# Kernel optimization log

Hardware: AMD Instinct MI355X
Metric: run time of the kernel (lower is better)

The kernel has to match this reference:

```python
import jax, jax.numpy as jnp
import numpy as np

RES_SCALE = 1.0

def prelu(x, a):
    return jnp.maximum(x, 0) + a * jnp.minimum(x, 0)

def conv1x1_prelu(x, w, b, a):
    # x: [N,C,H,W], w: [O,C], b: [O]
    y = jnp.einsum('nchw,oc->nohw', x, w) + b[None, :, None, None]
    return prelu(y, a)

def setup_inputs() -> dict:
    key = jax.random.key(0)
    ks = jax.random.split(key, 5)
    N, C, H, W = 2, 128, 96, 96
    Cr = C // 2  # reduction = 2
    return {
        'x':  jax.random.normal(ks[0], (N, C, H, W), jnp.float32),
        'w1': jax.random.normal(ks[1], (Cr, C), jnp.float32) * (1.0 / np.sqrt(C)),
        'b1': jnp.zeros((Cr,), jnp.float32),
        'a1': jnp.asarray(0.25, jnp.float32),
        'w2': jax.random.normal(ks[2], (Cr, C), jnp.float32) * (1.0 / np.sqrt(C)),
        'b2': jnp.zeros((Cr,), jnp.float32),
        'a2': jnp.asarray(0.25, jnp.float32),
        'wa': jax.random.normal(ks[3], (C, C), jnp.float32) * (1.0 / np.sqrt(C)),
        'ba': jnp.zeros((C,), jnp.float32),
        'aa': jnp.asarray(0.25, jnp.float32),
    }

def reference(x, w1, b1, a1, w2, b2, a2, wa, ba, aa):
    N, C, H, W = x.shape
    q = conv1x1_prelu(x, w1, b1, a1)   # [N,Cr,H,W]
    k = conv1x1_prelu(x, w2, b2, a2)   # [N,Cr,H,W]
    v = conv1x1_prelu(x, wa, ba, aa)   # [N,C,H,W]
    Cr = q.shape[1]
    L = H * W
    q = q.transpose(0, 2, 3, 1).reshape(N, L, Cr)   # [N,L,Cr]
    k = k.reshape(N, Cr, L)                          # [N,Cr,L]
    score = jax.nn.softmax(jnp.matmul(q, k), axis=2)  # [N,L,L]
    v = v.reshape(N, C, L).transpose(0, 2, 1)        # [N,L,C]
    out = jnp.matmul(score, v)                        # [N,L,C]
    out = out.transpose(0, 2, 1).reshape(N, C, H, W)
    return out + RES_SCALE * x
```

## Files before the change

### kernel.cpp

```cpp
#include <hip/hip_runtime.h>

#define N_  2
#define C_  128
#define CR_ 64
#define H_  96
#define W_  96
#define L_  (H_*W_)
#define QBLK 128
#define KVBLK 64
#define NQB (L_/QBLK)
#define SPLITS 8
#define TILES_PER ((L_/KVBLK)/SPLITS)
#define NCHUNK (N_*NQB*SPLITS)
#define LOG2E 1.44269504088896f

typedef short bf16x8 __attribute__((ext_vector_type(8)));
typedef float f32x4  __attribute__((ext_vector_type(4)));

static __device__ __forceinline__ float exp2_fast(float x) {
    return __builtin_amdgcn_exp2f(x);
}

static __device__ __forceinline__ unsigned short f2bf(float f) {
    unsigned u = __builtin_bit_cast(unsigned, f);
    unsigned rounding = 0x7FFFu + ((u >> 16) & 1u);
    return (unsigned short)((u + rounding) >> 16);
}

static __device__ __forceinline__ unsigned cvt_pk_bf16(float lo, float hi) {
    unsigned r;
    asm("v_cvt_pk_bf16_f32 %0, %1, %2" : "=v"(r) : "v"(lo), "v"(hi));
    return r;
}

static __device__ __forceinline__ float bf2f(unsigned short s) {
    return __builtin_bit_cast(float, ((unsigned)s) << 16);
}

static __device__ __forceinline__ int sigma_(int r) {
    return (r & 0x23) | ((r & 0x0C) << 1) | ((r & 0x10) >> 2);
}

#define GLD16(G, Ld) __builtin_amdgcn_global_load_lds( \
    (const __attribute__((address_space(1))) void*)(G), \
    (__attribute__((address_space(3))) void*)(Ld), 16, 0, 0)

__global__ __launch_bounds__(256) void wconv_kernel(
    const float* __restrict__ w1, const float* __restrict__ b1, const float* __restrict__ a1,
    const float* __restrict__ w2, const float* __restrict__ b2, const float* __restrict__ a2,
    const float* __restrict__ wa, const float* __restrict__ ba, const float* __restrict__ aa,
    unsigned short* __restrict__ Wbf,
    float* __restrict__ bias, float* __restrict__ alpha, float* __restrict__ scale)
{
    const int idx = blockIdx.x * 256 + threadIdx.x;
    const int o = idx >> 7, k = idx & 127;
    float wv;
    if (o < 64)       wv = w1[o*C_ + k];
    else if (o < 128) wv = w2[(o-64)*C_ + k];
    else              wv = wa[(o-128)*C_ + k];
    Wbf[idx] = f2bf(wv);
    if (blockIdx.x == 0) {
        int t = threadIdx.x;
        float b, a, sc;
        if (t < 64)       { b = b1[t];       a = a1[0]; sc = LOG2E; }
        else if (t < 128) { b = b2[t-64];    a = a2[0]; sc = 1.0f; }
        else              { b = ba[t-128];   a = aa[0]; sc = 1.0f; }
        bias[t] = b; alpha[t] = a; scale[t] = sc;
    }
}

__global__ __launch_bounds__(256) void proj_mfma_kernel(
    const float* __restrict__ x,
    const unsigned short* __restrict__ Wbf,
    const float* __restrict__ bias,
    const float* __restrict__ alpha,
    const float* __restrict__ scale,
    unsigned short* __restrict__ qkv)
{
    __shared__ alignas(16) unsigned char xs[32 * 256];

    const int blk  = blockIdx.x;
    const int n    = blk / (L_/32);
    const int i0   = (blk % (L_/32)) * 32;
    const float* xb = x + (size_t)n * C_ * L_;
    const int tid  = threadIdx.x;
    const int wv_  = tid >> 6;
    const int lane = tid & 63;
    const int lhi  = lane >> 4;
    const int llo  = lane & 15;

    {
        const int i = lane & 31;
        const int g = lane >> 5;
        #pragma unroll
        for (int p = 0; p < 4; p++) {
            int c0 = (p*8 + wv_*2 + g) * 4;
            float v0 = xb[(size_t)(c0+0)*L_ + i0 + i];
            float v1 = xb[(size_t)(c0+1)*L_ + i0 + i];
            float v2 = xb[(size_t)(c0+2)*L_ + i0 + i];
            float v3 = xb[(size_t)(c0+3)*L_ + i0 + i];
            uint2 pk2;
            pk2.x = cvt_pk_bf16(v0, v1);
            pk2.y = cvt_pk_bf16(v2, v3);
            int byte = i*256 + ((((c0 >> 3) ^ (i & 7))) << 4) + (c0 & 7) * 2;
            *reinterpret_cast<uint2*>(xs + byte) = pk2;
        }
    }
    __syncthreads();

    bf16x8 xf[2][4];
    #pragma unroll
    for (int it = 0; it < 2; it++) {
        int i = it*16 + llo;
        #pragma unroll
        for (int ks = 0; ks < 4; ks++) {
            int byte = i*256 + (((ks*4 + lhi) ^ (i & 7)) << 4);
            xf[it][ks] = *reinterpret_cast<const bf16x8*>(xs + byte);
        }
    }

    unsigned short* q_t = qkv;
    unsigned short* k_t = qkv + (size_t)N_ * L_ * CR_;
    unsigned short* v   = qkv + (size_t)2 * N_ * L_ * CR_;
    unsigned short* qtb = q_t + (size_t)n * L_ * CR_;
    unsigned short* ktb = k_t + (size_t)n * L_ * CR_;
    unsigned short* vb  = v   + (size_t)n * C_ * L_;

    #pragma unroll
    for (int oo = 0; oo < 2; oo++) {
        const int ot = wv_*2 + oo;
        const unsigned short* wrow = Wbf + (size_t)(ot*16 + llo) * 128;
        bf16x8 wf[4];
        #pragma unroll
        for (int ks = 0; ks < 4; ks++)
            wf[ks] = *reinterpret_cast<const bf16x8*>(wrow + ks*32 + lhi*8);

        f32x4 acc[2];
        acc[0] = f32x4{0.f, 0.f, 0.f, 0.f};
        acc[1] = f32x4{0.f, 0.f, 0.f, 0.f};
        #pragma unroll
        for (int ks = 0; ks < 4; ks++) {
            acc[0] = __builtin_amdgcn_mfma_f32_16x16x32_bf16(wf[ks], xf[0][ks], acc[0], 0, 0, 0);
            acc[1] = __builtin_amdgcn_mfma_f32_16x16x32_bf16(wf[ks], xf[1][ks], acc[1], 0, 0, 0);
        }

        const int ob = ot*16 + lhi*4;
        const float4 b4 = *reinterpret_cast<const float4*>(bias  + ob);
        const float4 a4 = *reinterpret_cast<const float4*>(alpha + ob);
        const float4 s4 = *reinterpret_cast<const float4*>(scale + ob);
        unsigned short* dst = (ot < 4) ? qtb : ktb;
        const int col = (ot & 3)*16 + lhi*4;
        #pragma unroll
        for (int it = 0; it < 2; it++) {
            int i = i0 + it*16 + llo;
            float y0 = acc[it][0] + b4.x; y0 = (fmaxf(y0,0.f) + a4.x*fminf(y0,0.f))*s4.x;
            float y1 = acc[it][1] + b4.y; y1 = (fmaxf(y1,0.f) + a4.y*fminf(y1,0.f))*s4.y;
            float y2 = acc[it][2] + b4.z; y2 = (fmaxf(y2,0.f) + a4.z*fminf(y2,0.f))*s4.z;
            float y3 = acc[it][3] + b4.w; y3 = (fmaxf(y3,0.f) + a4.w*fminf(y3,0.f))*s4.w;
            uint2 pk2;
            pk2.x = cvt_pk_bf16(y0, y1);
            pk2.y = cvt_pk_bf16(y2, y3);
            *reinterpret_cast<uint2*>(dst + (size_t)i * CR_ + col) = pk2;
        }
    }

    #pragma unroll
    for (int oo = 0; oo < 2; oo++) {
        const int ot2 = wv_*2 + oo;
        const int op  = ot2*16 + llo;
        const unsigned short* wrow = Wbf + (size_t)(128 + op) * 128;
        bf16x8 wf[4];
        #pragma unroll
        for (int ks = 0; ks < 4; ks++)
            wf[ks] = *reinterpret_cast<const bf16x8*>(wrow + ks*32 + lhi*8);

        f32x4 acc[2];
        acc[0] = f32x4{0.f, 0.f, 0.f, 0.f};
        acc[1] = f32x4{0.f, 0.f, 0.f, 0.f};
        #pragma unroll
        for (int ks = 0; ks < 4; ks++) {
            acc[0] = __builtin_amdgcn_mfma_f32_16x16x32_bf16(xf[0][ks], wf[ks], acc[0], 0, 0, 0);
            acc[1] = __builtin_amdgcn_mfma_f32_16x16x32_bf16(xf[1][ks], wf[ks], acc[1], 0, 0, 0);
        }

        const float b = bias[128 + op];
        const float a = alpha[128 + op];
        #pragma unroll
        for (int it = 0; it < 2; it++) {
            float y0 = acc[it][0] + b; y0 = fmaxf(y0,0.f) + a*fminf(y0,0.f);
            float y1 = acc[it][1] + b; y1 = fmaxf(y1,0.f) + a*fminf(y1,0.f);
            float y2 = acc[it][2] + b; y2 = fmaxf(y2,0.f) + a*fminf(y2,0.f);
            float y3 = acc[it][3] + b; y3 = fmaxf(y3,0.f) + a*fminf(y3,0.f);
            uint2 pk2;
            pk2.x = cvt_pk_bf16(y0, y1);
            pk2.y = cvt_pk_bf16(y2, y3);
            *reinterpret_cast<uint2*>(vb + (size_t)op * L_ + i0 + it*16 + lhi*4) = pk2;
        }
    }
}

__global__ __launch_bounds__(256, 3) void attn_kernel(
    const unsigned short* __restrict__ qkv,
    unsigned short* __restrict__ o_part,
    float* __restrict__ l_part)
{
    __shared__ alignas(16) unsigned char kv_lds[2][24*1024];

    const unsigned short* q_t = qkv;
    const unsigned short* k_t = qkv + (size_t)N_ * L_ * CR_;
    const unsigned short* v   = qkv + (size_t)2 * N_ * L_ * CR_;

    const int blk  = blockIdx.x;
    const int n    = blk / (NQB * SPLITS);
    const int rem  = blk % (NQB * SPLITS);
    const int qbi  = rem / SPLITS;
    const int s    = rem % SPLITS;
    const int qb   = qbi * QBLK;
    const int tid  = threadIdx.x;
    const int wave = tid >> 6;
    const int lane = tid & 63;
    const int lhi  = lane >> 4;
    const int llo  = lane & 15;

    const int jb_beg = s * TILES_PER * KVBLK;
    const int jb_end = jb_beg + TILES_PER * KVBLK;

    const unsigned short* qtb = q_t + (size_t)n * L_ * CR_;
    const unsigned short* ktb = k_t + (size_t)n * L_ * CR_;
    const unsigned short* vb  = v   + (size_t)n * C_ * L_;

    bf16x8 qf[2][2];
    #pragma unroll
    for (int st = 0; st < 2; st++) {
        int row = qb + wave * 32 + st * 16 + llo;
        #pragma unroll
        for (int ks = 0; ks < 2; ks++)
            qf[st][ks] = *reinterpret_cast<const bf16x8*>(qtb + (size_t)row * CR_ + ks*32 + lhi*8);
    }

    bf16x8 ones_f;
    #pragma unroll
    for (int e = 0; e < 8; e++) ones_f[e] = (short)0x3F80;

    const int l8 = lane >> 3;
    const int l7 = (lane & 7) * 16;
    const int rho0 = wave*16 + l8;
    const int rho1 = rho0 + 8;
    const unsigned short* kbase0 = ktb + (size_t)sigma_(rho0) * CR_ + ((l7 ^ ((rho0 & 7) << 4)) >> 1);
    const unsigned short* kbase1 = ktb + (size_t)sigma_(rho1) * CR_ + ((l7 ^ ((rho1 & 7) << 4)) >> 1);
    const unsigned short* vbase[4];
    #pragma unroll
    for (int vt = 0; vt < 4; vt++) {
        int c = wave*32 + vt*8 + l8;
        vbase[vt] = vb + (size_t)c * L_ + ((l7 ^ (l8 << 4)) >> 1);
    }

    #define STAGE(b, jb_) do {                                                   \
        GLD16(kbase0 + (size_t)(jb_) * CR_, &kv_lds[b][(wave*2+0)*1024 + 0]);    \
        GLD16(kbase1 + (size_t)(jb_) * CR_, &kv_lds[b][(wave*2+1)*1024 + 0]);    \
        GLD16(vbase[0] + (jb_), &kv_lds[b][8192 + (wave*4+0)*1024]);             \
        GLD16(vbase[1] + (jb_), &kv_lds[b][8192 + (wave*4+1)*1024]);             \
        GLD16(vbase[2] + (jb_), &kv_lds[b][8192 + (wave*4+2)*1024]);             \
        GLD16(vbase[3] + (jb_), &kv_lds[b][8192 + (wave*4+3)*1024]);             \
    } while (0)

    f32x4 o_acc[2][8];
    #pragma unroll
    for (int st = 0; st < 2; st++)
        #pragma unroll
        for (int ct = 0; ct < 8; ct++) o_acc[st][ct] = f32x4{0.f, 0.f, 0.f, 0.f};
    f32x4 acc_l[2];
    acc_l[0] = f32x4{0.f, 0.f, 0.f, 0.f};
    acc_l[1] = f32x4{0.f, 0.f, 0.f, 0.f};

    int cur = 0;
    STAGE(0, jb_beg);
    __syncthreads();

    for (int jb = jb_beg; jb < jb_end; jb += KVBLK) {
        if (jb + KVBLK < jb_end) STAGE(cur ^ 1, jb + KVBLK);

        const unsigned char* kbuf = &kv_lds[cur][0];
        const unsigned char* vbuf = &kv_lds[cur][8192];

        f32x4 sacc[2][4];
        #pragma unroll
        for (int st = 0; st < 2; st++)
            #pragma unroll
            for (int jt = 0; jt < 4; jt++) sacc[st][jt] = f32x4{0.f, 0.f, 0.f, 0.f};
        __builtin_amdgcn_s_setprio(1);
        #pragma unroll
        for (int ks = 0; ks < 2; ks++) {
            #pragma unroll
            for (int jt = 0; jt < 4; jt++) {
                int rho  = jt*16 + llo;
                int colb = ks*64 + lhi*16;
                bf16x8 kf = *reinterpret_cast<const bf16x8*>(
                    kbuf + rho*128 + (colb ^ ((rho & 7) << 4)));
                sacc[0][jt] = __builtin_amdgcn_mfma_f32_16x16x32_bf16(kf, qf[0][ks], sacc[0][jt], 0, 0, 0);
                sacc[1][jt] = __builtin_amdgcn_mfma_f32_16x16x32_bf16(kf, qf[1][ks], sacc[1][jt], 0, 0, 0);
            }
        }
        __builtin_amdgcn_s_setprio(0);

        #pragma unroll
        for (int st = 0; st < 2; st++)
            #pragma unroll
            for (int jt = 0; jt < 4; jt++)
                #pragma unroll
                for (int r = 0; r < 4; r++)
                    sacc[st][jt][r] = exp2_fast(sacc[st][jt][r]);

        __builtin_amdgcn_s_setprio(1);
        #pragma unroll
        for (int ks = 0; ks < 2; ks++) {
            unsigned pw0[4], pw1[4];
            pw0[0] = cvt_pk_bf16(sacc[0][2*ks][0],   sacc[0][2*ks][1]);
            pw0[1] = cvt_pk_bf16(sacc[0][2*ks][2],   sacc[0][2*ks][3]);
            pw0[2] = cvt_pk_bf16(sacc[0][2*ks+1][0], sacc[0][2*ks+1][1]);
            pw0[3] = cvt_pk_bf16(sacc[0][2*ks+1][2], sacc[0][2*ks+1][3]);
            pw1[0] = cvt_pk_bf16(sacc[1][2*ks][0],   sacc[1][2*ks][1]);
            pw1[1] = cvt_pk_bf16(sacc[1][2*ks][2],   sacc[1][2*ks][3]);
            pw1[2] = cvt_pk_bf16(sacc[1][2*ks+1][0], sacc[1][2*ks+1][1]);
            pw1[3] = cvt_pk_bf16(sacc[1][2*ks+1][2], sacc[1][2*ks+1][3]);
            bf16x8 pf0 = *reinterpret_cast<const bf16x8*>(&pw0[0]);
            bf16x8 pf1 = *reinterpret_cast<const bf16x8*>(&pw1[0]);
            acc_l[0] = __builtin_amdgcn_mfma_f32_16x16x32_bf16(ones_f, pf0, acc_l[0], 0, 0, 0);
            acc_l[1] = __builtin_amdgcn_mfma_f32_16x16x32_bf16(ones_f, pf1, acc_l[1], 0, 0, 0);
            #pragma unroll
            for (int ct = 0; ct < 8; ct++) {
                int c = ct*16 + llo;
                int colb = ks*64 + lhi*16;
                bf16x8 vf = *reinterpret_cast<const bf16x8*>(
                    vbuf + c*128 + (colb ^ ((c & 7) << 4)));
                o_acc[0][ct] = __builtin_amdgcn_mfma_f32_16x16x32_bf16(vf, pf0, o_acc[0][ct], 0, 0, 0);
                o_acc[1][ct] = __builtin_amdgcn_mfma_f32_16x16x32_bf16(vf, pf1, o_acc[1][ct], 0, 0, 0);
            }
        }
        __builtin_amdgcn_s_setprio(0);

        __syncthreads();
        cur ^= 1;
    }
    #undef STAGE

    unsigned short* ob = o_part + (size_t)blk * (QBLK*C_);
    float* lb = l_part + (size_t)blk * QBLK;
    #pragma unroll
    for (int st = 0; st < 2; st++) {
        int i_loc = wave*32 + st*16 + llo;
        #pragma unroll
        for (int ct = 0; ct < 8; ct++) {
            int c0 = ct*16 + lhi*4;
            uint2 pkd;
            pkd.x = cvt_pk_bf16(o_acc[st][ct][0], o_acc[st][ct][1]);
            pkd.y = cvt_pk_bf16(o_acc[st][ct][2], o_acc[st][ct][3]);
            *reinterpret_cast<uint2*>(ob + (size_t)i_loc * C_ + c0) = pkd;
        }
        if (lhi == 0) lb[i_loc] = acc_l[st][0];
    }
}

__global__ __launch_bounds__(256) void combine_kernel(
    const unsigned short* __restrict__ o_part,
    const float* __restrict__ l_part,
    const float* __restrict__ x,
    float* __restrict__ out)
{
    __shared__ float invl[32];

    const int blk  = blockIdx.x;
    const int part = blk & 3;
    const int qbi  = (blk >> 2) % NQB;
    const int n    = blk / (4 * NQB);
    const int tid  = threadIdx.x;
    const int i0   = part * 32;

    const size_t pbase = (size_t)(n*NQB + qbi) * SPLITS;

    if (tid < 32) {
        float lt = 0.f;
        for (int s = 0; s < SPLITS; s++)
            lt += l_part[(pbase + s) * QBLK + i0 + tid];
        invl[tid] = 1.0f / lt;
    }
    __syncthreads();

    const int il = tid & 31;
    const int cg = tid >> 5;

    float acc[16];
    #pragma unroll
    for (int k = 0; k < 16; k++) acc[k] = 0.f;

    for (int s = 0; s < SPLITS; s++) {
        const unsigned short* src = o_part + (pbase + s) * (QBLK*C_)
                                  + (size_t)(i0 + il) * C_ + cg*16;
        bf16x8 v0 = *reinterpret_cast<const bf16x8*>(src);
        bf16x8 v1 = *reinterpret_cast<const bf16x8*>(src + 8);
        #pragma unroll
        for (int k = 0; k < 8; k++) acc[k]     += bf2f((unsigned short)v0[k]);
        #pragma unroll
        for (int k = 0; k < 8; k++) acc[8 + k] += bf2f((unsigned short)v1[k]);
    }

    const float nv = invl[il];
    const int ig = qbi*QBLK + i0 + il;
    const float* xb = x   + (size_t)n * C_ * L_;
    float*       ob = out + (size_t)n * C_ * L_;
    #pragma unroll
    for (int k = 0; k < 16; k++) {
        int c = cg*16 + k;
        ob[(size_t)c * L_ + ig] = acc[k] * nv + xb[(size_t)c * L_ + ig];
    }
}

extern "C" void kernel_launch(void* const* d_in, const int* in_sizes, int n_in,
                              void* d_out, int out_size, void* d_ws, size_t ws_size,
                              hipStream_t stream) {
    const float* x  = (const float*)d_in[0];
    const float* w1 = (const float*)d_in[1];
    const float* b1 = (const float*)d_in[2];
    const float* a1 = (const float*)d_in[3];
    const float* w2 = (const float*)d_in[4];
    const float* b2 = (const float*)d_in[5];
    const float* a2 = (const float*)d_in[6];
    const float* wa = (const float*)d_in[7];
    const float* ba = (const float*)d_in[8];
    const float* aa = (const float*)d_in[9];
    float* out = (float*)d_out;

    unsigned short* qkv = (unsigned short*)d_ws;
    size_t qkv_bytes = ((size_t)2*N_*L_*CR_ + (size_t)N_*C_*L_) * 2;
    size_t off = (qkv_bytes + 255) & ~(size_t)255;

    unsigned short* o_part = (unsigned short*)((char*)d_ws + off);
    size_t o_elems = (size_t)NCHUNK * QBLK * C_;
    float* l_part = (float*)(o_part + o_elems);
    float* tail   = l_part + (size_t)NCHUNK * QBLK;
    unsigned short* Wbf = (unsigned short*)tail;
    float* bias  = (float*)(Wbf + 256*128);
    float* alpha = bias + 256;
    float* scale = alpha + 256;

    wconv_kernel<<<128, 256, 0, stream>>>(w1, b1, a1, w2, b2, a2, wa, ba, aa,
                                          Wbf, bias, alpha, scale);
    proj_mfma_kernel<<<N_ * (L_/32), 256, 0, stream>>>(x, Wbf, bias, alpha, scale, qkv);
    attn_kernel<<<NCHUNK, 256, 0, stream>>>(qkv, o_part, l_part);
    combine_kernel<<<N_ * NQB * 4, 256, 0, stream>>>(o_part, l_part, x, out);
}
```

Baseline: 99.33 us.

## Double query tile per block to reuse staged K/V across more rows

Raises the query block from 128 to 256 rows, so each wave handles 64 query rows and every K/V tile loaded into LDS feeds twice as many MFMAs. The score loop is restructured to go per key tile, doing exp2 and bf16 packing right after each score MFMA, which keeps fewer live fp32 score registers. The combine kernel is adjusted to the new block count. In exchange, register pressure roughly doubles for the output accumulators, occupancy drops from 3 to 2 blocks per CU, and the grid is halved, so there are fewer blocks to spread over the CUs.

```diff
diff --git a/kernel.cpp b/kernel.cpp
--- a/kernel.cpp
+++ b/kernel.cpp
@@ -6,7 +6,7 @@
 #define H_  96
 #define W_  96
 #define L_  (H_*W_)
-#define QBLK 128
+#define QBLK 256
 #define KVBLK 64
 #define NQB (L_/QBLK)
 #define SPLITS 8
@@ -199,7 +199,7 @@
     }
 }
 
-__global__ __launch_bounds__(256, 3) void attn_kernel(
+__global__ __launch_bounds__(256, 2) void attn_kernel(
     const unsigned short* __restrict__ qkv,
     unsigned short* __restrict__ o_part,
     float* __restrict__ l_part)
@@ -229,10 +229,10 @@
     const unsigned short* ktb = k_t + (size_t)n * L_ * CR_;
     const unsigned short* vb  = v   + (size_t)n * C_ * L_;
 
-    bf16x8 qf[2][2];
-    #pragma unroll
-    for (int st = 0; st < 2; st++) {
-        int row = qb + wave * 32 + st * 16 + llo;
+    bf16x8 qf[4][2];
+    #pragma unroll
+    for (int st = 0; st < 4; st++) {
+        int row = qb + wave * 64 + st * 16 + llo;
         #pragma unroll
         for (int ks = 0; ks < 2; ks++)
             qf[st][ks] = *reinterpret_cast<const bf16x8*>(qtb + (size_t)row * CR_ + ks*32 + lhi*8);
@@ -264,14 +264,14 @@
         GLD16(vbase[3] + (jb_), &kv_lds[b][8192 + (wave*4+3)*1024]);             \
     } while (0)
 
-    f32x4 o_acc[2][8];
-    #pragma unroll
-    for (int st = 0; st < 2; st++)
+    f32x4 o_acc[4][8];
+    #pragma unroll
+    for (int st = 0; st < 4; st++)
         #pragma unroll
         for (int ct = 0; ct < 8; ct++) o_acc[st][ct] = f32x4{0.f, 0.f, 0.f, 0.f};
-    f32x4 acc_l[2];
-    acc_l[0] = f32x4{0.f, 0.f, 0.f, 0.f};
-    acc_l[1] = f32x4{0.f, 0.f, 0.f, 0.f};
+    f32x4 acc_l[4];
+    #pragma unroll
+    for (int st = 0; st < 4; st++) acc_l[st] = f32x4{0.f, 0.f, 0.f, 0.f};
 
     int cur = 0;
     STAGE(0, jb_beg);
@@ -283,58 +283,51 @@
         const unsigned char* kbuf = &kv_lds[cur][0];
         const unsigned char* vbuf = &kv_lds[cur][8192];
 
-        f32x4 sacc[2][4];
-        #pragma unroll
-        for (int st = 0; st < 2; st++)
+        unsigned pk[4][8];
+        __builtin_amdgcn_s_setprio(1);
+        #pragma unroll
+        for (int jt = 0; jt < 4; jt++) {
+            f32x4 sacc[4];
             #pragma unroll
-            for (int jt = 0; jt < 4; jt++) sacc[st][jt] = f32x4{0.f, 0.f, 0.f, 0.f};
-        __builtin_amdgcn_s_setprio(1);
-        #pragma unroll
-        for (int ks = 0; ks < 2; ks++) {
+            for (int st = 0; st < 4; st++) sacc[st] = f32x4{0.f, 0.f, 0.f, 0.f};
             #pragma unroll
-            for (int jt = 0; jt < 4; jt++) {
+            for (int ks = 0; ks < 2; ks++) {
                 int rho  = jt*16 + llo;
                 int colb = ks*64 + lhi*16;
                 bf16x8 kf = *reinterpret_cast<const bf16x8*>(
                     kbuf + rho*128 + (colb ^ ((rho & 7) << 4)));
-                sacc[0][jt] = __builtin_amdgcn_mfma_f32_16x16x32_bf16(kf, qf[0][ks], sacc[0][jt], 0, 0, 0);
-                sacc[1][jt] = __builtin_amdgcn_mfma_f32_16x16x32_bf16(kf, qf[1][ks], sacc[1][jt], 0, 0, 0);
+                #pragma unroll
+                for (int st = 0; st < 4; st++)
+                    sacc[st] = __builtin_amdgcn_mfma_f32_16x16x32_bf16(kf, qf[st][ks], sacc[st], 0, 0, 0);
             }
-        }
-        __builtin_amdgcn_s_setprio(0);
-
-        #pragma unroll
-        for (int st = 0; st < 2; st++)
             #pragma unroll
-            for (int jt = 0; jt < 4; jt++)
-                #pragma unroll
-                for (int r = 0; r < 4; r++)
-                    sacc[st][jt][r] = exp2_fast(sacc[st][jt][r]);
-
-        __builtin_amdgcn_s_setprio(1);
+            for (int st = 0; st < 4; st++) {
+                float p0 = exp2_fast(sacc[st][0]);
+                float p1 = exp2_fast(sacc[st][1]);
+                float p2 = exp2_fast(sacc[st][2]);
+                float p3 = exp2_fast(sacc[st][3]);
+                pk[st][jt*2 + 0] = cvt_pk_bf16(p0, p1);
+                pk[st][jt*2 + 1] = cvt_pk_bf16(p2, p3);
+            }
+        }
+
         #pragma unroll
         for (int ks = 0; ks < 2; ks++) {
-            unsigned pw0[4], pw1[4];
-            pw0[0] = cvt_pk_bf16(sacc[0][2*ks][0],   sacc[0][2*ks][1]);
-            pw0[1] = cvt_pk_bf16(sacc[0][2*ks][2],   sacc[0][2*ks][3]);
-            pw0[2] = cvt_pk_bf16(sacc[0][2*ks+1][0], sacc[0][2*ks+1][1]);
-            pw0[3] = cvt_pk_bf16(sacc[0][2*ks+1][2], sacc[0][2*ks+1][3]);
-            pw1[0] = cvt_pk_bf16(sacc[1][2*ks][0],   sacc[1][2*ks][1]);
-            pw1[1] = cvt_pk_bf16(sacc[1][2*ks][2],   sacc[1][2*ks][3]);
-            pw1[2] = cvt_pk_bf16(sacc[1][2*ks+1][0], sacc[1][2*ks+1][1]);
-            pw1[3] = cvt_pk_bf16(sacc[1][2*ks+1][2], sacc[1][2*ks+1][3]);
-            bf16x8 pf0 = *reinterpret_cast<const bf16x8*>(&pw0[0]);
-            bf16x8 pf1 = *reinterpret_cast<const bf16x8*>(&pw1[0]);
-            acc_l[0] = __builtin_amdgcn_mfma_f32_16x16x32_bf16(ones_f, pf0, acc_l[0], 0, 0, 0);
-            acc_l[1] = __builtin_amdgcn_mfma_f32_16x16x32_bf16(ones_f, pf1, acc_l[1], 0, 0, 0);
+            bf16x8 pf[4];
+            #pragma unroll
+            for (int st = 0; st < 4; st++) {
+                pf[st] = *reinterpret_cast<const bf16x8*>(&pk[st][4*ks]);
+                acc_l[st] = __builtin_amdgcn_mfma_f32_16x16x32_bf16(ones_f, pf[st], acc_l[st], 0, 0, 0);
+            }
             #pragma unroll
             for (int ct = 0; ct < 8; ct++) {
                 int c = ct*16 + llo;
                 int colb = ks*64 + lhi*16;
                 bf16x8 vf = *reinterpret_cast<const bf16x8*>(
                     vbuf + c*128 + (colb ^ ((c & 7) << 4)));
-                o_acc[0][ct] = __builtin_amdgcn_mfma_f32_16x16x32_bf16(vf, pf0, o_acc[0][ct], 0, 0, 0);
-                o_acc[1][ct] = __builtin_amdgcn_mfma_f32_16x16x32_bf16(vf, pf1, o_acc[1][ct], 0, 0, 0);
+                #pragma unroll
+                for (int st = 0; st < 4; st++)
+                    o_acc[st][ct] = __builtin_amdgcn_mfma_f32_16x16x32_bf16(vf, pf[st], o_acc[st][ct], 0, 0, 0);
             }
         }
         __builtin_amdgcn_s_setprio(0);
@@ -347,8 +340,8 @@
     unsigned short* ob = o_part + (size_t)blk * (QBLK*C_);
     float* lb = l_part + (size_t)blk * QBLK;
     #pragma unroll
-    for (int st = 0; st < 2; st++) {
-        int i_loc = wave*32 + st*16 + llo;
+    for (int st = 0; st < 4; st++) {
+        int i_loc = wave*64 + st*16 + llo;
         #pragma unroll
         for (int ct = 0; ct < 8; ct++) {
             int c0 = ct*16 + lhi*4;
@@ -370,9 +363,9 @@
     __shared__ float invl[32];
 
     const int blk  = blockIdx.x;
-    const int part = blk & 3;
-    const int qbi  = (blk >> 2) % NQB;
-    const int n    = blk / (4 * NQB);
+    const int part = blk & 7;
+    const int qbi  = (blk >> 3) % NQB;
+    const int n    = blk / (8 * NQB);
     const int tid  = threadIdx.x;
     const int i0   = part * 32;
 
@@ -447,5 +440,5 @@
                                           Wbf, bias, alpha, scale);
     proj_mfma_kernel<<<N_ * (L_/32), 256, 0, stream>>>(x, Wbf, bias, alpha, scale, qkv);
     attn_kernel<<<NCHUNK, 256, 0, stream>>>(qkv, o_part, l_part);
-    combine_kernel<<<N_ * NQB * 4, 256, 0, stream>>>(o_part, l_part, x, out);
-}
+    combine_kernel<<<N_ * NQB * 8, 256, 0, stream>>>(o_part, l_part, x, out);
+}
```

New measurement: 112.0 us. 12.8% more time.
